# Performance work log

Hardware: AMD Instinct MI355X
Metric: run time of the kernel (lower is better)

The kernel has to match this reference:

```python
import jax, jax.numpy as jnp
import numpy as np

N, E = 50000, 800000
IN_DIM, HID, ZDIM = 256, 128, 64
LN_EPS = 1e-5


def _layernorm(x, gamma, beta):
    mu = jnp.mean(x, axis=-1, keepdims=True)
    var = jnp.mean(jnp.square(x - mu), axis=-1, keepdims=True)
    return (x - mu) * jax.lax.rsqrt(var + LN_EPS) * gamma + beta


def _gcn_conv(h, src, dst, dinv, W, b):
    # h: (N, d_in) -> (N, d_out). GCNConv: X W, then sym-normalized
    # aggregation over edges with self-loops, then bias.
    h = h @ W                                   # (N, d_out)
    coef = dinv[src] * dinv[dst]                # (E,)
    agg = jax.ops.segment_sum(h[src] * coef[:, None], dst,
                              num_segments=h.shape[0])
    agg = agg + h * jnp.square(dinv)[:, None]   # self-loop term
    return agg + b


def setup_inputs() -> dict:
    key = jax.random.key(0)
    ks = jax.random.split(key, 5)
    x = jax.random.normal(ks[0], (N, IN_DIM), dtype=jnp.float32)
    edge_index = jax.random.randint(ks[1], (2, E), 0, N, dtype=jnp.int64)
    s1 = 1.0 / np.sqrt(IN_DIM)
    s2 = 1.0 / np.sqrt(HID)
    return {
        "x": x,
        "edge_index": edge_index,
        "ln_gamma": jnp.ones((IN_DIM,), jnp.float32),
        "ln_beta": jnp.zeros((IN_DIM,), jnp.float32),
        "W1": jax.random.normal(ks[2], (IN_DIM, HID), jnp.float32) * s1,
        "b1": jnp.zeros((HID,), jnp.float32),
        "W2": jax.random.normal(ks[3], (HID, HID), jnp.float32) * s2,
        "b2": jnp.zeros((HID,), jnp.float32),
        "W3": jax.random.normal(ks[4], (HID, ZDIM), jnp.float32) * s2,
        "b3": jnp.zeros((ZDIM,), jnp.float32),
    }


def reference(x, edge_index, ln_gamma, ln_beta, W1, b1, W2, b2, W3, b3):
    src, dst = edge_index[0], edge_index[1]
    n = x.shape[0]
    # degree with self-loops (dropout is inference no-op, training=False)
    deg = jnp.ones((n,), x.dtype).at[dst].add(1.0)
    dinv = jax.lax.rsqrt(deg)
    h = _layernorm(x, ln_gamma, ln_beta)
    h = jax.nn.relu(_gcn_conv(h, src, dst, dinv, W1, b1))
    h = jax.nn.relu(_gcn_conv(h, src, dst, dinv, W2, b2))
    z = _gcn_conv(h, src, dst, dinv, W3, b3)
    return z
```

## Files before the change

kernel.cpp:

```cpp
#include <hip/hip_runtime.h>
#include <cstdint>
#include <cstddef>


typedef __attribute__((ext_vector_type(8))) __bf16 bf16x8;
typedef __attribute__((ext_vector_type(4))) float f32x4;
typedef _Float16 half_t;
typedef __attribute__((ext_vector_type(8))) _Float16 half8_t;

#define NHIST 256

__global__ __launch_bounds__(256) void prep_misc(
    const int* __restrict__ dst,
    const float* __restrict__ W1, const float* __restrict__ W2,
    const float* __restrict__ W3,
    int* __restrict__ bcnt_multi,
    unsigned short* __restrict__ W1t_hi, unsigned short* __restrict__ W1t_lo,
    unsigned short* __restrict__ W2t_hi, unsigned short* __restrict__ W2t_lo,
    unsigned short* __restrict__ W3t_hi, unsigned short* __restrict__ W3t_lo,
    int E) {
  int blk = blockIdx.x;
  int tid = threadIdx.x;
  if (blk < NHIST) {
    __shared__ int h[256];
    h[tid] = 0;
    __syncthreads();
    for (int e = blk * 256 + tid; e < E; e += NHIST * 256)
      atomicAdd(&h[dst[e] >> 8], 1);
    __syncthreads();
    bcnt_multi[blk * 256 + tid] = h[tid];
    return;
  }
  int idx = (blk - NHIST) * 256 + tid;
  const float* W;
  unsigned short *Th, *Tl;
  int K, NOUT;
  if (idx < 32768) {
    W = W1; Th = W1t_hi; Tl = W1t_lo; K = 256; NOUT = 128;
  } else if (idx < 49152) {
    idx -= 32768;
    W = W2; Th = W2t_hi; Tl = W2t_lo; K = 128; NOUT = 128;
  } else {
    idx -= 49152;
    W = W3; Th = W3t_hi; Tl = W3t_lo; K = 128; NOUT = 64;
  }
  int k = idx / NOUT, c = idx % NOUT;
  float v = W[idx];
  __bf16 h = (__bf16)v;
  __bf16 l = (__bf16)(v - (float)h);
  Th[(size_t)c * K + k] = __builtin_bit_cast(unsigned short, h);
  Tl[(size_t)c * K + k] = __builtin_bit_cast(unsigned short, l);
}

__global__ __launch_bounds__(256) void scan_buckets(const int* __restrict__ bcnt_multi,
                                                    int* __restrict__ bbase,
                                                    int* __restrict__ bcur, int NB, int E) {
  __shared__ int tmp[256];
  int t = threadIdx.x;
  int v = 0;
  for (int h = 0; h < NHIST; ++h) v += bcnt_multi[h * 256 + t];
  tmp[t] = v;
  __syncthreads();
  for (int off = 1; off < 256; off <<= 1) {
    int x = (t >= off) ? tmp[t - off] : 0;
    __syncthreads();
    tmp[t] += x;
    __syncthreads();
  }
  int excl = tmp[t] - v;
  if (t < NB) { bbase[t] = excl; bcur[t] = excl; }
  if (t == 0) bbase[NB] = E;
}

#define CHUNK 4096
__global__ __launch_bounds__(256) void scatter_bins(const int* __restrict__ src,
                                                    const int* __restrict__ dst,
                                                    int* __restrict__ bcur,
                                                    unsigned int* __restrict__ binned, int E) {
  __shared__ unsigned int recs[CHUNK];
  __shared__ int hist[256], lbase[256], resv[256], cur[256];
  int t = threadIdx.x;
  int e0 = blockIdx.x * CHUNK;
  if (e0 >= E) return;
  int len = min(CHUNK, E - e0);
  hist[t] = 0;
  cur[t] = 0;
  __syncthreads();
  for (int i = t; i < len; i += 256) atomicAdd(&hist[dst[e0 + i] >> 8], 1);
  __syncthreads();
  int v = hist[t];
  lbase[t] = v;
  __syncthreads();
  for (int off = 1; off < 256; off <<= 1) {
    int x = (t >= off) ? lbase[t - off] : 0;
    __syncthreads();
    lbase[t] += x;
    __syncthreads();
  }
  int myexcl = lbase[t] - v;
  if (v) resv[t] = atomicAdd(&bcur[t], v);
  __syncthreads();
  lbase[t] = myexcl;
  __syncthreads();
  for (int i = t; i < len; i += 256) {
    int d = dst[e0 + i], s = src[e0 + i];
    int b = d >> 8;
    int r = atomicAdd(&cur[b], 1);
    recs[lbase[b] + r] = ((unsigned int)d << 16) | (unsigned int)s;
  }
  __syncthreads();
  for (int i = t; i < len; i += 256) {
    unsigned int rc = recs[i];
    int b = rc >> 24;
    binned[resv[b] + (i - lbase[b])] = rc;
  }
}

#define MAXB 8192
__global__ __launch_bounds__(256) void sort_bucket(const unsigned int* __restrict__ binned,
                                                   const int* __restrict__ bbase,
                                                   int* __restrict__ srcs,
                                                   int* __restrict__ offs,
                                                   float* __restrict__ dinv,
                                                   int N, int NB, int E) {
  __shared__ int sstage[MAXB];
  __shared__ int hist[256], nbase[256], cur[256], tmp[256];
  int b = blockIdx.x, t = threadIdx.x;
  int base = bbase[b], end = bbase[b + 1];
  int L = end - base;
  if (L > MAXB) L = MAXB;
  hist[t] = 0;
  __syncthreads();
  for (int i = t; i < L; i += 256)
    atomicAdd(&hist[(binned[base + i] >> 16) & 255], 1);
  __syncthreads();
  int v = hist[t];
  tmp[t] = v;
  __syncthreads();
  for (int off = 1; off < 256; off <<= 1) {
    int x = (t >= off) ? tmp[t - off] : 0;
    __syncthreads();
    tmp[t] += x;
    __syncthreads();
  }
  int excl = tmp[t] - v;
  nbase[t] = excl;
  cur[t] = excl;
  int node = (b << 8) + t;
  if (node < N) {
    offs[node] = base + excl;
    dinv[node] = rsqrtf(1.0f + (float)v);
  }
  if (b == NB - 1 && t == 0) offs[N] = E;
  __syncthreads();
  for (int i = t; i < L; i += 256) {
    unsigned int p = binned[base + i];
    int ld = (p >> 16) & 255;
    int slot = atomicAdd(&cur[ld], 1);
    sstage[slot] = (int)(p & 0xFFFFu);
  }
  __syncthreads();
  for (int i = t; i < L; i += 256) srcs[base + i] = sstage[i];
}

template <int K, int NOUT, bool LN, bool A_FP16>
__launch_bounds__(256)
__global__ void gemm_mfma(const void* __restrict__ Avoid,
                          const unsigned short* __restrict__ Wt_hi,
                          const unsigned short* __restrict__ Wt_lo,
                          const float* __restrict__ gamma, const float* __restrict__ beta,
                          half_t* __restrict__ out, int nrows) {
  constexpr int BM = 64, BK = 32;
  constexpr int NT = NOUT / 16;
  __shared__ unsigned short As_hi[BM][BK];
  __shared__ unsigned short As_lo[BM][BK];
  __shared__ unsigned short Bs_hi[NOUT][BK];
  __shared__ unsigned short Bs_lo[NOUT][BK];
  __shared__ float mu_s[BM];
  __shared__ float rs_s[BM];

  const int tid = threadIdx.x;
  const int lane = tid & 63;
  const int w = tid >> 6;
  const int quad = lane >> 4;
  const int l16 = lane & 15;
  const int row0 = blockIdx.x * BM;

  if (LN) {
    const float* A = (const float*)Avoid;
    int r = tid >> 2;
    int part = tid & 3;
    int grow = row0 + r;
    if (grow > nrows - 1) grow = nrows - 1;
    const float4* rp = (const float4*)(A + (size_t)grow * K);
    float s = 0.f, s2 = 0.f;
#pragma unroll
    for (int j = 0; j < K / 16; ++j) {
      float4 v = rp[part * (K / 16) + j];
      s += v.x + v.y + v.z + v.w;
      s2 += v.x * v.x + v.y * v.y + v.z * v.z + v.w * v.w;
    }
    s += __shfl_xor(s, 1);
    s += __shfl_xor(s, 2);
    s2 += __shfl_xor(s2, 1);
    s2 += __shfl_xor(s2, 2);
    if (part == 0) {
      float m = s * (1.0f / (float)K);
      float var = s2 * (1.0f / (float)K) - m * m;
      mu_s[r] = m;
      rs_s[r] = rsqrtf(var + 1e-5f);
    }
    __syncthreads();
  }

  f32x4 acc[NT];
#pragma unroll
  for (int t = 0; t < NT; ++t) acc[t] = (f32x4){0.f, 0.f, 0.f, 0.f};

  for (int k0 = 0; k0 < K; k0 += BK) {
    if (!A_FP16) {
      const float* A = (const float*)Avoid;
#pragma unroll
      for (int i = 0; i < 2; ++i) {
        int r = i * 32 + (tid >> 3);
        int c4 = (tid & 7) * 4;
        int grow = row0 + r;
        if (grow > nrows - 1) grow = nrows - 1;
        float4 v = *(const float4*)&A[(size_t)grow * K + k0 + c4];
        if (LN) {
          float m = mu_s[r], s = rs_s[r];
          float4 g = *(const float4*)&gamma[k0 + c4];
          float4 b = *(const float4*)&beta[k0 + c4];
          v.x = (v.x - m) * s * g.x + b.x;
          v.y = (v.y - m) * s * g.y + b.y;
          v.z = (v.z - m) * s * g.z + b.z;
          v.w = (v.w - m) * s * g.w + b.w;
        }
        float vv[4] = {v.x, v.y, v.z, v.w};
#pragma unroll
        for (int j = 0; j < 4; ++j) {
          __bf16 h = (__bf16)vv[j];
          __bf16 l = (__bf16)(vv[j] - (float)h);
          As_hi[r][c4 + j] = __builtin_bit_cast(unsigned short, h);
          As_lo[r][c4 + j] = __builtin_bit_cast(unsigned short, l);
        }
      }
    } else {
      const half_t* A = (const half_t*)Avoid;
      int r = tid >> 2;
      int c8 = (tid & 3) * 8;
      int grow = row0 + r;
      if (grow > nrows - 1) grow = nrows - 1;
      half8_t v = *(const half8_t*)&A[(size_t)grow * K + k0 + c8];
#pragma unroll
      for (int j = 0; j < 8; ++j) {
        float f = (float)v[j];
        __bf16 h = (__bf16)f;
        __bf16 l = (__bf16)(f - (float)h);
        As_hi[r][c8 + j] = __builtin_bit_cast(unsigned short, h);
        As_lo[r][c8 + j] = __builtin_bit_cast(unsigned short, l);
      }
    }
#pragma unroll
    for (int i = 0; i < NOUT / 64; ++i) {
      int n = i * 64 + (tid >> 2);
      int c8 = (tid & 3) * 8;
      *(uint4*)&Bs_hi[n][c8] = *(const uint4*)&Wt_hi[(size_t)n * K + k0 + c8];
      *(uint4*)&Bs_lo[n][c8] = *(const uint4*)&Wt_lo[(size_t)n * K + k0 + c8];
    }
    __syncthreads();

    bf16x8 ah = *(const bf16x8*)&As_hi[w * 16 + l16][quad * 8];
    bf16x8 al = *(const bf16x8*)&As_lo[w * 16 + l16][quad * 8];
#pragma unroll
    for (int t = 0; t < NT; ++t) {
      bf16x8 bh = *(const bf16x8*)&Bs_hi[t * 16 + l16][quad * 8];
      bf16x8 bl = *(const bf16x8*)&Bs_lo[t * 16 + l16][quad * 8];
      acc[t] = __builtin_amdgcn_mfma_f32_16x16x32_bf16(ah, bh, acc[t], 0, 0, 0);
      acc[t] = __builtin_amdgcn_mfma_f32_16x16x32_bf16(al, bh, acc[t], 0, 0, 0);
      acc[t] = __builtin_amdgcn_mfma_f32_16x16x32_bf16(ah, bl, acc[t], 0, 0, 0);
    }
    __syncthreads();
  }

#pragma unroll
  for (int t = 0; t < NT; ++t) {
#pragma unroll
    for (int r = 0; r < 4; ++r) {
      int grow = row0 + w * 16 + quad * 4 + r;
      if (grow < nrows) out[(size_t)grow * NOUT + t * 16 + l16] = (half_t)acc[t][r];
    }
  }
}

__global__ __launch_bounds__(256) void agg128_h(const half_t* __restrict__ t,
                                                const int* __restrict__ offs,
                                                const int* __restrict__ srcs,
                                                const float* __restrict__ dinv,
                                                const float* __restrict__ bias,
                                                half_t* __restrict__ out, int n) {
  int gid = blockIdx.x * blockDim.x + threadIdx.x;
  int node = gid >> 6, lane = gid & 63;
  if (node >= n) return;
  int qw = lane >> 4;
  int fl = lane & 15;
  int e0 = offs[node], e1 = offs[node + 1];
  float acc[8] = {0.f, 0.f, 0.f, 0.f, 0.f, 0.f, 0.f, 0.f};
  int e = e0 + qw;
  for (; e + 12 < e1; e += 16) {
    int sa = srcs[e], sb = srcs[e + 4], sc = srcs[e + 8], sd = srcs[e + 12];
    float wa = dinv[sa], wb = dinv[sb], wc = dinv[sc], wd = dinv[sd];
    half8_t va = *(const half8_t*)(t + ((size_t)sa << 7) + fl * 8);
    half8_t vb = *(const half8_t*)(t + ((size_t)sb << 7) + fl * 8);
    half8_t vc = *(const half8_t*)(t + ((size_t)sc << 7) + fl * 8);
    half8_t vd = *(const half8_t*)(t + ((size_t)sd << 7) + fl * 8);
#pragma unroll
    for (int j = 0; j < 8; ++j) {
      acc[j] = fmaf(wa, (float)va[j], acc[j]);
      acc[j] = fmaf(wb, (float)vb[j], acc[j]);
      acc[j] = fmaf(wc, (float)vc[j], acc[j]);
      acc[j] = fmaf(wd, (float)vd[j], acc[j]);
    }
  }
  for (; e < e1; e += 4) {
    int s = srcs[e];
    float w = dinv[s];
    half8_t v = *(const half8_t*)(t + ((size_t)s << 7) + fl * 8);
#pragma unroll
    for (int j = 0; j < 8; ++j) acc[j] = fmaf(w, (float)v[j], acc[j]);
  }
#pragma unroll
  for (int j = 0; j < 8; ++j) {
    acc[j] += __shfl_xor(acc[j], 16);
    acc[j] += __shfl_xor(acc[j], 32);
  }
  if (qw == 0) {
    float di = dinv[node];
    float dii = di * di;
    half8_t sv = *(const half8_t*)(t + ((size_t)node << 7) + fl * 8);
    float4 b0 = *(const float4*)(bias + fl * 8);
    float4 b1 = *(const float4*)(bias + fl * 8 + 4);
    float bb[8] = {b0.x, b0.y, b0.z, b0.w, b1.x, b1.y, b1.z, b1.w};
    half8_t o;
#pragma unroll
    for (int j = 0; j < 8; ++j) {
      float v = di * acc[j] + dii * (float)sv[j] + bb[j];
      o[j] = (half_t)fmaxf(v, 0.f);
    }
    *(half8_t*)(out + ((size_t)node << 7) + fl * 8) = o;
  }
}

__global__ __launch_bounds__(256) void agg64_h(const half_t* __restrict__ t,
                                               const int* __restrict__ offs,
                                               const int* __restrict__ srcs,
                                               const float* __restrict__ dinv,
                                               const float* __restrict__ bias,
                                               float* __restrict__ out, int n) {
  int gid = blockIdx.x * blockDim.x + threadIdx.x;
  int node = gid >> 6, lane = gid & 63;
  if (node >= n) return;
  int og = lane >> 3;
  int fl = lane & 7;
  int e0 = offs[node], e1 = offs[node + 1];
  float acc[8] = {0.f, 0.f, 0.f, 0.f, 0.f, 0.f, 0.f, 0.f};
  int e = e0 + og;
  for (; e + 8 < e1; e += 16) {
    int sa = srcs[e], sb = srcs[e + 8];
    float wa = dinv[sa], wb = dinv[sb];
    half8_t va = *(const half8_t*)(t + ((size_t)sa << 6) + fl * 8);
    half8_t vb = *(const half8_t*)(t + ((size_t)sb << 6) + fl * 8);
#pragma unroll
    for (int j = 0; j < 8; ++j) {
      acc[j] = fmaf(wa, (float)va[j], acc[j]);
      acc[j] = fmaf(wb, (float)vb[j], acc[j]);
    }
  }
  for (; e < e1; e += 8) {
    int s = srcs[e];
    float w = dinv[s];
    half8_t v = *(const half8_t*)(t + ((size_t)s << 6) + fl * 8);
#pragma unroll
    for (int j = 0; j < 8; ++j) acc[j] = fmaf(w, (float)v[j], acc[j]);
  }
#pragma unroll
  for (int j = 0; j < 8; ++j) {
    acc[j] += __shfl_xor(acc[j], 8);
    acc[j] += __shfl_xor(acc[j], 16);
    acc[j] += __shfl_xor(acc[j], 32);
  }
  if (og == 0) {
    float di = dinv[node];
    float dii = di * di;
    half8_t sv = *(const half8_t*)(t + ((size_t)node << 6) + fl * 8);
    float4 b0 = *(const float4*)(bias + fl * 8);
    float4 b1 = *(const float4*)(bias + fl * 8 + 4);
    float bb[8] = {b0.x, b0.y, b0.z, b0.w, b1.x, b1.y, b1.z, b1.w};
    float ov[8];
#pragma unroll
    for (int j = 0; j < 8; ++j) ov[j] = di * acc[j] + dii * (float)sv[j] + bb[j];
    *(float4*)(out + ((size_t)node << 6) + fl * 8) = make_float4(ov[0], ov[1], ov[2], ov[3]);
    *(float4*)(out + ((size_t)node << 6) + fl * 8 + 4) = make_float4(ov[4], ov[5], ov[6], ov[7]);
  }
}

extern "C" void kernel_launch(void* const* d_in, const int* in_sizes, int n_in,
                              void* d_out, int out_size, void* d_ws, size_t ws_size,
                              hipStream_t stream) {
  const float* x = (const float*)d_in[0];
  const int* ei = (const int*)d_in[1];
  const float* gamma = (const float*)d_in[2];
  const float* beta = (const float*)d_in[3];
  const float* W1 = (const float*)d_in[4];
  const float* b1 = (const float*)d_in[5];
  const float* W2 = (const float*)d_in[6];
  const float* b2 = (const float*)d_in[7];
  const float* W3 = (const float*)d_in[8];
  const float* b3 = (const float*)d_in[9];
  float* out = (float*)d_out;

  const int N = in_sizes[0] / 256;
  const int E = in_sizes[1] / 2;
  const int* src = ei;
  const int* dst = ei + E;
  const int NB = (N + 255) >> 8;

  char* ws = (char*)d_ws;
  auto alloc = [&](size_t bytes) -> char* {
    char* p = ws;
    ws += (bytes + 255) & ~(size_t)255;
    return p;
  };
  int* bcnt_multi = (int*)alloc(NHIST * 256 * 4);
  int* bbase = (int*)alloc(257 * 4);
  int* bcur = (int*)alloc(256 * 4);
  unsigned int* binned = (unsigned int*)alloc((size_t)E * 4);
  int* srcs = (int*)alloc((size_t)E * 4);
  int* offs = (int*)alloc((size_t)(N + 1) * 4);
  float* dinv = (float*)alloc((size_t)N * 4);
  half_t* t = (half_t*)alloc((size_t)N * 128 * 2);
  half_t* h = (half_t*)alloc((size_t)N * 128 * 2);
  unsigned short* W1t_hi = (unsigned short*)alloc(256 * 128 * 2);
  unsigned short* W1t_lo = (unsigned short*)alloc(256 * 128 * 2);
  unsigned short* W2t_hi = (unsigned short*)alloc(128 * 128 * 2);
  unsigned short* W2t_lo = (unsigned short*)alloc(128 * 128 * 2);
  unsigned short* W3t_hi = (unsigned short*)alloc(128 * 64 * 2);
  unsigned short* W3t_lo = (unsigned short*)alloc(128 * 64 * 2);

  prep_misc<<<NHIST + 224, 256, 0, stream>>>(
      dst, W1, W2, W3, bcnt_multi, W1t_hi, W1t_lo, W2t_hi, W2t_lo,
      W3t_hi, W3t_lo, E);

  scan_buckets<<<1, 256, 0, stream>>>(bcnt_multi, bbase, bcur, NB, E);
  scatter_bins<<<(E + CHUNK - 1) / CHUNK, 256, 0, stream>>>(src, dst, bcur, binned, E);
  sort_bucket<<<NB, 256, 0, stream>>>(binned, bbase, srcs, offs, dinv, N, NB, E);

  const int gemm_blocks = (N + 63) / 64;
  const int agg_blocks = (N + 3) / 4;

  gemm_mfma<256, 128, true, false><<<gemm_blocks, 256, 0, stream>>>(
      x, W1t_hi, W1t_lo, gamma, beta, t, N);
  agg128_h<<<agg_blocks, 256, 0, stream>>>(t, offs, srcs, dinv, b1, h, N);

  gemm_mfma<128, 128, false, true><<<gemm_blocks, 256, 0, stream>>>(
      h, W2t_hi, W2t_lo, nullptr, nullptr, t, N);
  agg128_h<<<agg_blocks, 256, 0, stream>>>(t, offs, srcs, dinv, b2, h, N);

  gemm_mfma<128, 64, false, true><<<gemm_blocks, 256, 0, stream>>>(
      h, W3t_hi, W3t_lo, nullptr, nullptr, t, N);
  agg64_h<<<agg_blocks, 256, 0, stream>>>(t, offs, srcs, dinv, b3, out, N);
}
```

Baseline: 282.0 us.

## Co-schedule GEMM1 halves with edge scatter and bucket sort kernels, pad LDS rows

Merges the edge scatter and bucket sort kernels each with half of the first LayerNorm+GEMM blocks, so independent graph preprocessing and dense work share launches and fill the GPU together. Shared memory becomes a raw buffer carved per role. The GEMM LDS tiles also gain a padded row stride (BK+8) to cut bank conflicts on the MFMA operand reads. The cost is higher LDS per block from the union layout, which may reduce occupancy, and uneven block workloads within each launch.

```diff
diff --git a/kernel.cpp b/kernel.cpp
--- a/kernel.cpp
+++ b/kernel.cpp
@@ -9,6 +9,8 @@
 typedef __attribute__((ext_vector_type(8))) _Float16 half8_t;
 
 #define NHIST 256
+#define CHUNK 4096
+#define MAXB 8192
 
 __global__ __launch_bounds__(256) void prep_misc(
     const int* __restrict__ dst,
@@ -72,15 +74,18 @@
   if (t == 0) bbase[NB] = E;
 }
 
-#define CHUNK 4096
-__global__ __launch_bounds__(256) void scatter_bins(const int* __restrict__ src,
-                                                    const int* __restrict__ dst,
-                                                    int* __restrict__ bcur,
-                                                    unsigned int* __restrict__ binned, int E) {
-  __shared__ unsigned int recs[CHUNK];
-  __shared__ int hist[256], lbase[256], resv[256], cur[256];
+__device__ __forceinline__ void scatter_body(char* smem_raw, int bid,
+                                             const int* __restrict__ src,
+                                             const int* __restrict__ dst,
+                                             int* __restrict__ bcur,
+                                             unsigned int* __restrict__ binned, int E) {
+  unsigned int* recs = (unsigned int*)smem_raw;
+  int* hist = (int*)(smem_raw + 16384);
+  int* lbase = hist + 256;
+  int* resv = lbase + 256;
+  int* cur = resv + 256;
   int t = threadIdx.x;
-  int e0 = blockIdx.x * CHUNK;
+  int e0 = bid * CHUNK;
   if (e0 >= E) return;
   int len = min(CHUNK, E - e0);
   hist[t] = 0;
@@ -116,16 +121,19 @@
   }
 }
 
-#define MAXB 8192
-__global__ __launch_bounds__(256) void sort_bucket(const unsigned int* __restrict__ binned,
-                                                   const int* __restrict__ bbase,
-                                                   int* __restrict__ srcs,
-                                                   int* __restrict__ offs,
-                                                   float* __restrict__ dinv,
-                                                   int N, int NB, int E) {
-  __shared__ int sstage[MAXB];
-  __shared__ int hist[256], nbase[256], cur[256], tmp[256];
-  int b = blockIdx.x, t = threadIdx.x;
+__device__ __forceinline__ void sort_body(char* smem_raw, int b,
+                                          const unsigned int* __restrict__ binned,
+                                          const int* __restrict__ bbase,
+                                          int* __restrict__ srcs,
+                                          int* __restrict__ offs,
+                                          float* __restrict__ dinv,
+                                          int N, int NB, int E) {
+  int* sstage = (int*)smem_raw;
+  int* hist = (int*)(smem_raw + 32768);
+  int* nbase = hist + 256;
+  int* cur = nbase + 256;
+  int* tmp = cur + 256;
+  int t = threadIdx.x;
   int base = bbase[b], end = bbase[b + 1];
   int L = end - base;
   if (L > MAXB) L = MAXB;
@@ -164,29 +172,30 @@
 }
 
 template <int K, int NOUT, bool LN, bool A_FP16>
-__launch_bounds__(256)
-__global__ void gemm_mfma(const void* __restrict__ Avoid,
-                          const unsigned short* __restrict__ Wt_hi,
-                          const unsigned short* __restrict__ Wt_lo,
-                          const float* __restrict__ gamma, const float* __restrict__ beta,
-                          half_t* __restrict__ out, int nrows) {
-  constexpr int BM = 64, BK = 32;
+__device__ __forceinline__ void gemm_body(char* smem_raw, int gbid,
+                                          const void* __restrict__ Avoid,
+                                          const unsigned short* __restrict__ Wt_hi,
+                                          const unsigned short* __restrict__ Wt_lo,
+                                          const float* __restrict__ gamma,
+                                          const float* __restrict__ beta,
+                                          half_t* __restrict__ out, int nrows) {
+  constexpr int BM = 64, BK = 32, BKP = BK + 8;
   constexpr int NT = NOUT / 16;
-  __shared__ unsigned short As_hi[BM][BK];
-  __shared__ unsigned short As_lo[BM][BK];
-  __shared__ unsigned short Bs_hi[NOUT][BK];
-  __shared__ unsigned short Bs_lo[NOUT][BK];
-  __shared__ float mu_s[BM];
-  __shared__ float rs_s[BM];
+  unsigned short* As_hi = (unsigned short*)smem_raw;
+  unsigned short* As_lo = As_hi + BM * BKP;
+  unsigned short* Bs_hi = As_lo + BM * BKP;
+  unsigned short* Bs_lo = Bs_hi + NOUT * BKP;
+  float* mu_s = (float*)(Bs_lo + NOUT * BKP);
+  float* rs_s = mu_s + BM;
 
   const int tid = threadIdx.x;
   const int lane = tid & 63;
   const int w = tid >> 6;
   const int quad = lane >> 4;
   const int l16 = lane & 15;
-  const int row0 = blockIdx.x * BM;
-
-  if (LN) {
+  const int row0 = gbid * BM;
+
+  if constexpr (LN) {
     const float* A = (const float*)Avoid;
     int r = tid >> 2;
     int part = tid & 3;
@@ -218,7 +227,7 @@
   for (int t = 0; t < NT; ++t) acc[t] = (f32x4){0.f, 0.f, 0.f, 0.f};
 
   for (int k0 = 0; k0 < K; k0 += BK) {
-    if (!A_FP16) {
+    if constexpr (!A_FP16) {
       const float* A = (const float*)Avoid;
 #pragma unroll
       for (int i = 0; i < 2; ++i) {
@@ -227,7 +236,7 @@
         int grow = row0 + r;
         if (grow > nrows - 1) grow = nrows - 1;
         float4 v = *(const float4*)&A[(size_t)grow * K + k0 + c4];
-        if (LN) {
+        if constexpr (LN) {
           float m = mu_s[r], s = rs_s[r];
           float4 g = *(const float4*)&gamma[k0 + c4];
           float4 b = *(const float4*)&beta[k0 + c4];
@@ -241,8 +250,8 @@
         for (int j = 0; j < 4; ++j) {
           __bf16 h = (__bf16)vv[j];
           __bf16 l = (__bf16)(vv[j] - (float)h);
-          As_hi[r][c4 + j] = __builtin_bit_cast(unsigned short, h);
-          As_lo[r][c4 + j] = __builtin_bit_cast(unsigned short, l);
+          As_hi[r * BKP + c4 + j] = __builtin_bit_cast(unsigned short, h);
+          As_lo[r * BKP + c4 + j] = __builtin_bit_cast(unsigned short, l);
         }
       }
     } else {
@@ -257,25 +266,25 @@
         float f = (float)v[j];
         __bf16 h = (__bf16)f;
         __bf16 l = (__bf16)(f - (float)h);
-        As_hi[r][c8 + j] = __builtin_bit_cast(unsigned short, h);
-        As_lo[r][c8 + j] = __builtin_bit_cast(unsigned short, l);
+        As_hi[r * BKP + c8 + j] = __builtin_bit_cast(unsigned short, h);
+        As_lo[r * BKP + c8 + j] = __builtin_bit_cast(unsigned short, l);
       }
     }
 #pragma unroll
     for (int i = 0; i < NOUT / 64; ++i) {
       int n = i * 64 + (tid >> 2);
       int c8 = (tid & 3) * 8;
-      *(uint4*)&Bs_hi[n][c8] = *(const uint4*)&Wt_hi[(size_t)n * K + k0 + c8];
-      *(uint4*)&Bs_lo[n][c8] = *(const uint4*)&Wt_lo[(size_t)n * K + k0 + c8];
-    }
-    __syncthreads();
-
-    bf16x8 ah = *(const bf16x8*)&As_hi[w * 16 + l16][quad * 8];
-    bf16x8 al = *(const bf16x8*)&As_lo[w * 16 + l16][quad * 8];
+      *(uint4*)&Bs_hi[n * BKP + c8] = *(const uint4*)&Wt_hi[(size_t)n * K + k0 + c8];
+      *(uint4*)&Bs_lo[n * BKP + c8] = *(const uint4*)&Wt_lo[(size_t)n * K + k0 + c8];
+    }
+    __syncthreads();
+
+    bf16x8 ah = *(const bf16x8*)&As_hi[(w * 16 + l16) * BKP + quad * 8];
+    bf16x8 al = *(const bf16x8*)&As_lo[(w * 16 + l16) * BKP + quad * 8];
 #pragma unroll
     for (int t = 0; t < NT; ++t) {
-      bf16x8 bh = *(const bf16x8*)&Bs_hi[t * 16 + l16][quad * 8];
-      bf16x8 bl = *(const bf16x8*)&Bs_lo[t * 16 + l16][quad * 8];
+      bf16x8 bh = *(const bf16x8*)&Bs_hi[(t * 16 + l16) * BKP + quad * 8];
+      bf16x8 bl = *(const bf16x8*)&Bs_lo[(t * 16 + l16) * BKP + quad * 8];
       acc[t] = __builtin_amdgcn_mfma_f32_16x16x32_bf16(ah, bh, acc[t], 0, 0, 0);
       acc[t] = __builtin_amdgcn_mfma_f32_16x16x32_bf16(al, bh, acc[t], 0, 0, 0);
       acc[t] = __builtin_amdgcn_mfma_f32_16x16x32_bf16(ah, bl, acc[t], 0, 0, 0);
@@ -291,6 +300,49 @@
       if (grow < nrows) out[(size_t)grow * NOUT + t * 16 + l16] = (half_t)acc[t][r];
     }
   }
+}
+
+__global__ __launch_bounds__(256) void fused_scatter_gemm1(
+    const int* __restrict__ src, const int* __restrict__ dst,
+    int* __restrict__ bcur, unsigned int* __restrict__ binned, int E,
+    const float* __restrict__ x,
+    const unsigned short* __restrict__ W1t_hi, const unsigned short* __restrict__ W1t_lo,
+    const float* __restrict__ gamma, const float* __restrict__ beta,
+    half_t* __restrict__ t, int nrows, int nscat) {
+  __shared__ __align__(16) char smem[31232];
+  if ((int)blockIdx.x < nscat)
+    scatter_body(smem, blockIdx.x, src, dst, bcur, binned, E);
+  else
+    gemm_body<256, 128, true, false>(smem, blockIdx.x - nscat, x, W1t_hi, W1t_lo,
+                                     gamma, beta, t, nrows);
+}
+
+__global__ __launch_bounds__(256) void fused_sort_gemm1(
+    const unsigned int* __restrict__ binned, const int* __restrict__ bbase,
+    int* __restrict__ srcs, int* __restrict__ offs, float* __restrict__ dinv,
+    int N, int NB, int E,
+    const float* __restrict__ x,
+    const unsigned short* __restrict__ W1t_hi, const unsigned short* __restrict__ W1t_lo,
+    const float* __restrict__ gamma, const float* __restrict__ beta,
+    half_t* __restrict__ t, int nrows, int g1a) {
+  __shared__ __align__(16) char smem[36864];
+  if ((int)blockIdx.x < NB)
+    sort_body(smem, blockIdx.x, binned, bbase, srcs, offs, dinv, N, NB, E);
+  else
+    gemm_body<256, 128, true, false>(smem, g1a + (blockIdx.x - NB), x, W1t_hi, W1t_lo,
+                                     gamma, beta, t, nrows);
+}
+
+template <int K, int NOUT>
+__launch_bounds__(256)
+__global__ void gemm_k(const half_t* __restrict__ A,
+                       const unsigned short* __restrict__ Wt_hi,
+                       const unsigned short* __restrict__ Wt_lo,
+                       half_t* __restrict__ out, int nrows) {
+  constexpr int SM = 64 * 40 * 4 + NOUT * 40 * 4 + 512;
+  __shared__ __align__(16) char smem[SM];
+  gemm_body<K, NOUT, false, true>(smem, blockIdx.x, A, Wt_hi, Wt_lo,
+                                  nullptr, nullptr, out, nrows);
 }
 
 __global__ __launch_bounds__(256) void agg128_h(const half_t* __restrict__ t,
@@ -452,21 +504,25 @@
       W3t_hi, W3t_lo, E);
 
   scan_buckets<<<1, 256, 0, stream>>>(bcnt_multi, bbase, bcur, NB, E);
-  scatter_bins<<<(E + CHUNK - 1) / CHUNK, 256, 0, stream>>>(src, dst, bcur, binned, E);
-  sort_bucket<<<NB, 256, 0, stream>>>(binned, bbase, srcs, offs, dinv, N, NB, E);
 
   const int gemm_blocks = (N + 63) / 64;
+  const int G1A = gemm_blocks / 2;
+  const int G1B = gemm_blocks - G1A;
+  const int NSCAT = (E + CHUNK - 1) / CHUNK;
   const int agg_blocks = (N + 3) / 4;
 
-  gemm_mfma<256, 128, true, false><<<gemm_blocks, 256, 0, stream>>>(
-      x, W1t_hi, W1t_lo, gamma, beta, t, N);
+  fused_scatter_gemm1<<<NSCAT + G1A, 256, 0, stream>>>(
+      src, dst, bcur, binned, E, x, W1t_hi, W1t_lo, gamma, beta, t, N, NSCAT);
+
+  fused_sort_gemm1<<<NB + G1B, 256, 0, stream>>>(
+      binned, bbase, srcs, offs, dinv, N, NB, E, x, W1t_hi, W1t_lo, gamma, beta,
+      t, N, G1A);
+
   agg128_h<<<agg_blocks, 256, 0, stream>>>(t, offs, srcs, dinv, b1, h, N);
 
-  gemm_mfma<128, 128, false, true><<<gemm_blocks, 256, 0, stream>>>(
-      h, W2t_hi, W2t_lo, nullptr, nullptr, t, N);
+  gemm_k<128, 128><<<gemm_blocks, 256, 0, stream>>>(h, W2t_hi, W2t_lo, t, N);
   agg128_h<<<agg_blocks, 256, 0, stream>>>(t, offs, srcs, dinv, b2, h, N);
 
-  gemm_mfma<128, 64, false, true><<<gemm_blocks, 256, 0, stream>>>(
-      h, W3t_hi, W3t_lo, nullptr, nullptr, t, N);
+  gemm_k<128, 64><<<gemm_blocks, 256, 0, stream>>>(h, W3t_hi, W3t_lo, t, N);
   agg64_h<<<agg_blocks, 256, 0, stream>>>(t, offs, srcs, dinv, b3, out, N);
 }
```

Result: faster. 271.5 us (-3.7%).
